# Kernel tuning notes

Measured on AMD Instinct MI355X. Metric: run time of the kernel, lower is better.

Reference implementation:

```python
import jax, jax.numpy as jnp
import numpy as np

N_STATES = 64   # n_dice
N_OBS = 128     # number of distinct roll values (rows of log_likelihood table)
T = 262144      # sequence length


def setup_inputs() -> dict:
    key = jax.random.key(0)
    k1, k2, k3 = jax.random.split(key, 3)
    rolls = jax.random.randint(k1, (T,), 0, N_OBS)
    # torch.nn.init.normal(param, -1, 0.1): mean -1, std 0.1
    transition = jax.random.normal(k2, (N_STATES, N_STATES + 1), dtype=jnp.float32) * 0.1 - 1.0
    # emission log-likelihood table [n_obs, n_states]
    loglik_table = jax.nn.log_softmax(
        jax.random.normal(k3, (N_OBS, N_STATES), dtype=jnp.float32), axis=0)
    return {"rolls": rolls, "transition": transition, "loglik_table": loglik_table}


def reference(rolls, transition, loglik_table):
    """Viterbi decode: returns (path, final_score).

    Faithful to CRF.forward / _viterbi_algorithm, including the quirk that the
    emission vector ll_t is added along the PREVIOUS-state axis
    (roll.view(1,-1) broadcast over prev states), and that the returned path is
    in reverse-time order [s_{T-1}, ..., s_0].
    """
    S = transition.shape[0]
    ll = loglik_table[rolls]                 # [T, S]
    trans = transition[:, :S]                # [S, S]  (next, prev)
    init_delta = transition[:, S] + ll[0]    # [S]     start scores

    def step(delta, ll_t):
        # scores[next, prev] = trans[next, prev] + ll_t[prev] + delta[prev]
        scores = trans + (ll_t + delta)[None, :]
        bp = jnp.argmax(scores, axis=1)      # [S] backpointers
        return jnp.max(scores, axis=1), bp

    final_delta, bps = jax.lax.scan(step, init_delta, ll[1:])  # bps: [T-1, S]
    final_state = jnp.argmax(final_delta)
    final_score = final_delta[final_state]

    def back(state, bp_t):
        prev = bp_t[state]
        return prev, prev

    # reverse-time backtrack; ys[t] = decoded state at time t (t = 0..T-2)
    _, ys = jax.lax.scan(back, final_state, bps, reverse=True)
    path = jnp.concatenate([final_state[None], ys[::-1]])  # [s_{T-1},...,s_0]
    return path, final_score
```

## Files before the change

kernel.cpp:

```cpp
#include <hip/hip_runtime.h>
#include <hip/hip_fp16.h>
#include <stdint.h>

#define T_LEN 262144
#define S 64
#define SP1 65

#define L_FWD 32
#define W_FWD 4
#define NSTEP (L_FWD + W_FWD)
#define C_FWD (T_LEN / L_FWD)

#define LB2 8
#define VB2 8
#define NW (T_LEN / LB2)
#define PITCH (LB2 + 2)

template <int CTRL>
__device__ __forceinline__ float dpp_fmax_step(float v) {
    int t = __builtin_amdgcn_update_dpp(__float_as_int(v), __float_as_int(v),
                                        CTRL, 0xf, 0xf, false);
    return fmaxf(__int_as_float(t), v);
}
template <int CTRL>
__device__ __forceinline__ unsigned int dpp_umin_step(unsigned int v) {
    unsigned int t = (unsigned int)__builtin_amdgcn_update_dpp(
        (int)v, (int)v, CTRL, 0xf, 0xf, false);
    return t < v ? t : v;
}

__device__ __forceinline__ float readlane_f(float v, int lane) {
    return __int_as_float(__builtin_amdgcn_readlane(__float_as_int(v), lane));
}

__device__ __forceinline__ unsigned int pack_key(float a, int j) {
    return (__float_as_uint(a) & 0xFFFFFFC0u) | (unsigned)j;
}

__global__ __launch_bounds__(512, 8) void k1_forward(
    const int* __restrict__ rolls, const float* __restrict__ trans,
    const float* __restrict__ ll,
    unsigned int* __restrict__ bp4, int* __restrict__ wsFinal,
    float* __restrict__ out_score) {
    __shared__ float strans[S * S];
    __shared__ __half sll[128 * S];
    const int tid = threadIdx.x;
    const int lane = tid & 63;
    const int wv = tid >> 6;

    if (blockIdx.x == 0 && tid == 0)
        out_score[0] = 0.0f;

    for (int k = tid; k < S * S; k += 512) {
        int i = k >> 6, j = k & 63;
        strans[(j << 6) | i] = trans[i * SP1 + j];
    }
    for (int k = tid; k < 128 * S; k += 512)
        sll[k] = __float2half(ll[k]);

    float rm = 3.0e38f;
    #pragma unroll
    for (int w = 0; w < S; ++w)
        rm = fminf(rm, trans[lane * SP1 + w]);
    float mc = 3.0e38f;
    #pragma unroll
    for (int i = 0; i < S; ++i)
        mc = fminf(mc, readlane_f(rm, i) - trans[i * SP1 + lane]);
    const float mcol = mc - 0.01f;
    __syncthreads();

    const int c = blockIdx.x * 8 + wv;
    const int t0 = c * L_FWD - W_FWD;

    int vroll = rolls[min(max(t0 + lane, 0), T_LEN - 1)];

    float delta = 0.0f;
    unsigned int pk[8];
    const int lane4 = lane << 0;

    #pragma unroll
    for (int st = 0; st < NSTEP; ++st) {
        int r = __builtin_amdgcn_readlane(vroll, st);
        float llv = __half2float(sll[(r << 6) | lane]);

        float cvec = delta + llv;

        float mxc = cvec;
        mxc = dpp_fmax_step<0x111>(mxc);
        mxc = dpp_fmax_step<0x112>(mxc);
        mxc = dpp_fmax_step<0x114>(mxc);
        mxc = dpp_fmax_step<0x118>(mxc);
        mxc = dpp_fmax_step<0x142>(mxc);
        mxc = dpp_fmax_step<0x143>(mxc);
        float cmax = readlane_f(mxc, 63);

        float thr = cmax + mcol;
        unsigned long long m0 = __ballot(cvec >= thr);

        int j0 = __ffsll(m0) - 1;
        unsigned long long m1 = m0 & (m0 - 1);
        int j1 = m1 ? (__ffsll(m1) - 1) : j0;
        unsigned long long m2 = m1 & (m1 - 1);
        int j2 = m2 ? (__ffsll(m2) - 1) : j0;
        unsigned long long m3 = m2 & (m2 - 1);
        int j3 = m3 ? (__ffsll(m3) - 1) : j0;

        float a0 = strans[(j0 << 6) | lane] + readlane_f(cvec, j0);
        float a1 = strans[(j1 << 6) | lane] + readlane_f(cvec, j1);
        float a2 = strans[(j2 << 6) | lane] + readlane_f(cvec, j2);
        float a3 = strans[(j3 << 6) | lane] + readlane_f(cvec, j3);

        unsigned int m = min(min(pack_key(a0, j0), pack_key(a1, j1)),
                             min(pack_key(a2, j2), pack_key(a3, j3)));

        delta = __uint_as_float(m & 0xFFFFFFC0u);

        if (st >= W_FWD) {
            int q = (st - W_FWD) >> 2, u = (st - W_FWD) & 3;
            if (u == 0) pk[q] = (m & 63u);
            else        pk[q] |= (m & 63u) << (8 * u);
        }
    }

    const int qb = c * (L_FWD / 4);
    #pragma unroll
    for (int q = 0; q < 8; ++q)
        bp4[(unsigned)((qb + q) << 6) | (unsigned)lane] = pk[q];

    if (c == C_FWD - 1) {
        unsigned int key = __float_as_uint(delta) | (unsigned)lane;
        key = dpp_umin_step<0x111>(key);
        key = dpp_umin_step<0x112>(key);
        key = dpp_umin_step<0x114>(key);
        key = dpp_umin_step<0x118>(key);
        key = dpp_umin_step<0x142>(key);
        key = dpp_umin_step<0x143>(key);
        unsigned int kall = (unsigned int)__builtin_amdgcn_readlane((int)key, 63);
        if (lane == 0)
            *wsFinal = (int)(kall & 63u);
    }
    (void)lane4;
}

__global__ __launch_bounds__(256) void k2_backtrack(
    const unsigned int* __restrict__ bp4, const int* __restrict__ wsFinal,
    const int* __restrict__ rolls, const float* __restrict__ trans,
    const float* __restrict__ ll, float* __restrict__ out_path,
    float* __restrict__ out_score) {
    __shared__ int sst[256 * PITCH];
    __shared__ float spart[4];
    const int tid = threadIdx.x;
    const int b = blockIdx.x * 256 + tid;
    const int tlo = b * LB2;
    const int thi = tlo + LB2 - 1;
    int te = thi + VB2;
    int s;
    if (te >= T_LEN - 1) {
        te = T_LEN - 1;
        s = *wsFinal;
    } else {
        s = 0;
    }
    int* row = sst + tid * PITCH;
    #pragma unroll
    for (int u = 0; u < LB2 + VB2 - 1; ++u) {
        int t = te - u;
        if (t > tlo) {
            if (t <= thi + 1) row[t - tlo] = s;
            unsigned int w = bp4[((unsigned)(t >> 2) << 6) | (unsigned)s];
            s = (int)((w >> ((t & 3) << 3)) & 63u);
        }
    }
    row[0] = s;
    __syncthreads();

    #pragma unroll
    for (int u = 0; u < LB2; ++u)
        out_path[T_LEN - 1 - (tlo + u)] = (float)row[u];

    float acc = 0.0f;
    #pragma unroll
    for (int u = 1; u <= LB2; ++u) {
        int t = tlo + u;
        if (t <= T_LEN - 1) {
            int sp = row[u - 1];
            int st = (u == LB2)
                         ? ((tid < 255) ? sst[(tid + 1) * PITCH] : row[LB2])
                         : row[u];
            acc += trans[st * SP1 + sp] + ll[rolls[t] * S + sp];
        }
    }
    if (b == 0) {
        int s0 = row[0];
        acc += trans[s0 * SP1 + S] + ll[rolls[0] * S + s0];
    }

    for (int off = 32; off; off >>= 1)
        acc += __shfl_xor(acc, off);
    if ((tid & 63) == 0) spart[tid >> 6] = acc;
    __syncthreads();
    if (tid == 0)
        atomicAdd(out_score, (spart[0] + spart[1]) + (spart[2] + spart[3]));
}

extern "C" void kernel_launch(void* const* d_in, const int* in_sizes, int n_in,
                              void* d_out, int out_size, void* d_ws, size_t ws_size,
                              hipStream_t stream) {
    const int* rolls = (const int*)d_in[0];
    const float* trans = (const float*)d_in[1];
    const float* ll = (const float*)d_in[2];
    float* out = (float*)d_out;
    char* ws = (char*)d_ws;
    int* wsFinal = (int*)(ws + 8);
    unsigned int* bp4 = (unsigned int*)(ws + 2048);

    k1_forward<<<C_FWD / 8, 512, 0, stream>>>(rolls, trans, ll, bp4, wsFinal,
                                              out + T_LEN);
    k2_backtrack<<<NW / 256, 256, 0, stream>>>(bp4, wsFinal, rolls, trans, ll,
                                               out, out + T_LEN);
}
```

Before: 114.5 us.

## Fuse pairs of Viterbi steps via precomputed per-roll max-plus two-step matrices

Adds a precompute kernel that builds, for each of the 128 roll values, a combined two-step max-plus transition matrix and a per-column pruning threshold. The forward pass then advances two time steps per iteration, halving the sequential chain length, and reads the combined matrices from global memory instead of LDS. The backtrack recovers the skipped intermediate states by an argmax over the middle state. In exchange it adds a 2 MB table built every call, global-memory gathers inside the forward loop, and a wave-wide reduction per recovered state in the backtrack.

```diff
diff --git a/kernel.cpp b/kernel.cpp
--- a/kernel.cpp
+++ b/kernel.cpp
@@ -5,16 +5,14 @@
 #define T_LEN 262144
 #define S 64
 #define SP1 65
-
-#define L_FWD 32
-#define W_FWD 4
-#define NSTEP (L_FWD + W_FWD)
-#define C_FWD (T_LEN / L_FWD)
-
-#define LB2 8
-#define VB2 8
-#define NW (T_LEN / LB2)
-#define PITCH (LB2 + 2)
+#define NCT 131072
+
+#define L_C 16
+#define W_C 4
+#define NSTEP (L_C + W_C)
+#define C_FWD (NCT / L_C)
+
+#define NW2 (T_LEN / 16)
 
 template <int CTRL>
 __device__ __forceinline__ float dpp_fmax_step(float v) {
@@ -28,62 +26,110 @@
         (int)v, (int)v, CTRL, 0xf, 0xf, false);
     return t < v ? t : v;
 }
-
 __device__ __forceinline__ float readlane_f(float v, int lane) {
     return __int_as_float(__builtin_amdgcn_readlane(__float_as_int(v), lane));
 }
-
 __device__ __forceinline__ unsigned int pack_key(float a, int j) {
     return (__float_as_uint(a) & 0xFFFFFFC0u) | (unsigned)j;
 }
-
-__global__ __launch_bounds__(512, 8) void k1_forward(
+__device__ __forceinline__ unsigned int wave_umin(unsigned int key) {
+    key = dpp_umin_step<0x111>(key);
+    key = dpp_umin_step<0x112>(key);
+    key = dpp_umin_step<0x114>(key);
+    key = dpp_umin_step<0x118>(key);
+    key = dpp_umin_step<0x142>(key);
+    key = dpp_umin_step<0x143>(key);
+    return (unsigned int)__builtin_amdgcn_readlane((int)key, 63);
+}
+
+__global__ __launch_bounds__(1024) void k0_m2(
+    const float* __restrict__ trans, const float* __restrict__ ll,
+    float* __restrict__ wsM2col, float* __restrict__ wsMc2,
+    float* __restrict__ out_score) {
+    __shared__ float sR[S * S];
+    __shared__ float sC[S * S];
+    __shared__ float sv[S];
+    __shared__ float sM2[S * S];
+    __shared__ float srm[S];
+    const int r = blockIdx.x, tid = threadIdx.x;
+    const int lane = tid & 63, wv = tid >> 6;
+    for (int k = tid; k < S * S; k += 1024) {
+        float v = trans[(k >> 6) * SP1 + (k & 63)];
+        sR[k] = v;
+        sC[k] = v;
+    }
+    if (tid < S) sv[tid] = ll[r * S + tid];
+    __syncthreads();
+    #pragma unroll
+    for (int ii = 0; ii < 4; ++ii) {
+        int i = wv * 4 + ii;
+        float m = -3.0e38f;
+        for (int k = 0; k < S; ++k) {
+            float tik = sR[(i << 6) | k] + sv[k];
+            m = fmaxf(m, tik + sC[(k << 6) | lane]);
+        }
+        sM2[(i << 6) | lane] = m;
+    }
+    __syncthreads();
+    if (tid < S) {
+        float rm = 3.0e38f;
+        for (int j = 0; j < S; ++j) rm = fminf(rm, sM2[(tid << 6) | j]);
+        srm[tid] = rm;
+    }
+    __syncthreads();
+    if (tid < S) {
+        float mc = 3.0e38f;
+        for (int i = 0; i < S; ++i) mc = fminf(mc, srm[i] - sM2[(i << 6) | tid]);
+        wsMc2[r * S + tid] = mc;
+    }
+    for (int idx = tid; idx < S * S; idx += 1024) {
+        int j = idx >> 6, i = idx & 63;
+        wsM2col[(r << 12) | idx] = sM2[(i << 6) | j];
+    }
+    if (r == 0 && tid == 0) out_score[0] = 0.0f;
+}
+
+__global__ __launch_bounds__(256, 8) void k1_forward(
     const int* __restrict__ rolls, const float* __restrict__ trans,
-    const float* __restrict__ ll,
-    unsigned int* __restrict__ bp4, int* __restrict__ wsFinal,
-    float* __restrict__ out_score) {
-    __shared__ float strans[S * S];
+    const float* __restrict__ ll, const float* __restrict__ wsMc2,
+    const float* __restrict__ wsM2col, unsigned int* __restrict__ bp4,
+    int* __restrict__ wsFinal, unsigned char* __restrict__ bpF) {
     __shared__ __half sll[128 * S];
     const int tid = threadIdx.x;
     const int lane = tid & 63;
     const int wv = tid >> 6;
 
-    if (blockIdx.x == 0 && tid == 0)
-        out_score[0] = 0.0f;
-
-    for (int k = tid; k < S * S; k += 512) {
-        int i = k >> 6, j = k & 63;
-        strans[(j << 6) | i] = trans[i * SP1 + j];
-    }
-    for (int k = tid; k < 128 * S; k += 512)
+    for (int k = tid; k < 128 * S; k += 256)
         sll[k] = __float2half(ll[k]);
-
-    float rm = 3.0e38f;
-    #pragma unroll
-    for (int w = 0; w < S; ++w)
-        rm = fminf(rm, trans[lane * SP1 + w]);
-    float mc = 3.0e38f;
-    #pragma unroll
-    for (int i = 0; i < S; ++i)
-        mc = fminf(mc, readlane_f(rm, i) - trans[i * SP1 + lane]);
-    const float mcol = mc - 0.01f;
-    __syncthreads();
-
-    const int c = blockIdx.x * 8 + wv;
-    const int t0 = c * L_FWD - W_FWD;
-
-    int vroll = rolls[min(max(t0 + lane, 0), T_LEN - 1)];
+    __syncthreads();
+
+    const int c = blockIdx.x * 4 + wv;
+    const int ct0 = c * L_C - W_C;
+
+    int ci = ct0 + lane;
+    int vrO = rolls[min(max(2 * ci + 1, 0), T_LEN - 1)];
+    int vrE = rolls[min(max(2 * ci + 2, 0), T_LEN - 1)];
 
     float delta = 0.0f;
-    unsigned int pk[8];
-    const int lane4 = lane << 0;
+    unsigned int pk[4];
+    float dsave = 0.0f;
+
+    int rO0 = __builtin_amdgcn_readlane(vrO, 0);
+    int rE0 = __builtin_amdgcn_readlane(vrE, 0);
+    float ll_cur = __half2float(sll[(rO0 << 6) | lane]);
+    float mc_cur = wsMc2[(rE0 << 6) | lane];
 
     #pragma unroll
     for (int st = 0; st < NSTEP; ++st) {
-        int r = __builtin_amdgcn_readlane(vroll, st);
-        float llv = __half2float(sll[(r << 6) | lane]);
-
-        float cvec = delta + llv;
+        int rO_n = __builtin_amdgcn_readlane(vrO, st + 1);
+        int rE_n = __builtin_amdgcn_readlane(vrE, st + 1);
+        float ll_nxt = __half2float(sll[(rO_n << 6) | lane]);
+        float mc_nxt = wsMc2[(rE_n << 6) | lane];
+        int rE = __builtin_amdgcn_readlane(vrE, st);
+
+        if (st == NSTEP - 1) dsave = delta;
+
+        float cvec = delta + ll_cur;
 
         float mxc = cvec;
         mxc = dpp_fmax_step<0x111>(mxc);
@@ -94,7 +140,7 @@
         mxc = dpp_fmax_step<0x143>(mxc);
         float cmax = readlane_f(mxc, 63);
 
-        float thr = cmax + mcol;
+        float thr = cmax + mc_cur;
         unsigned long long m0 = __ballot(cvec >= thr);
 
         int j0 = __ffsll(m0) - 1;
@@ -105,99 +151,126 @@
         unsigned long long m3 = m2 & (m2 - 1);
         int j3 = m3 ? (__ffsll(m3) - 1) : j0;
 
-        float a0 = strans[(j0 << 6) | lane] + readlane_f(cvec, j0);
-        float a1 = strans[(j1 << 6) | lane] + readlane_f(cvec, j1);
-        float a2 = strans[(j2 << 6) | lane] + readlane_f(cvec, j2);
-        float a3 = strans[(j3 << 6) | lane] + readlane_f(cvec, j3);
+        const float* base = wsM2col + ((size_t)rE << 12);
+        float a0 = base[(j0 << 6) | lane] + readlane_f(cvec, j0);
+        float a1 = base[(j1 << 6) | lane] + readlane_f(cvec, j1);
+        float a2 = base[(j2 << 6) | lane] + readlane_f(cvec, j2);
+        float a3 = base[(j3 << 6) | lane] + readlane_f(cvec, j3);
 
         unsigned int m = min(min(pack_key(a0, j0), pack_key(a1, j1)),
                              min(pack_key(a2, j2), pack_key(a3, j3)));
 
         delta = __uint_as_float(m & 0xFFFFFFC0u);
 
-        if (st >= W_FWD) {
-            int q = (st - W_FWD) >> 2, u = (st - W_FWD) & 3;
+        if (st >= W_C) {
+            int q = (st - W_C) >> 2, u = (st - W_C) & 3;
             if (u == 0) pk[q] = (m & 63u);
             else        pk[q] |= (m & 63u) << (8 * u);
         }
-    }
-
-    const int qb = c * (L_FWD / 4);
-    #pragma unroll
-    for (int q = 0; q < 8; ++q)
+        ll_cur = ll_nxt;
+        mc_cur = mc_nxt;
+    }
+
+    const int qb = c * 4;
+    #pragma unroll
+    for (int q = 0; q < 4; ++q)
         bp4[(unsigned)((qb + q) << 6) | (unsigned)lane] = pk[q];
 
     if (c == C_FWD - 1) {
-        unsigned int key = __float_as_uint(delta) | (unsigned)lane;
-        key = dpp_umin_step<0x111>(key);
-        key = dpp_umin_step<0x112>(key);
-        key = dpp_umin_step<0x114>(key);
-        key = dpp_umin_step<0x118>(key);
-        key = dpp_umin_step<0x142>(key);
-        key = dpp_umin_step<0x143>(key);
-        unsigned int kall = (unsigned int)__builtin_amdgcn_readlane((int)key, 63);
+        int rF = rolls[T_LEN - 1];
+        float cvF = dsave + __half2float(sll[(rF << 6) | lane]);
+        unsigned int mbest = 0xFFFFFFFFu;
+        for (int j = 0; j < S; ++j) {
+            float a = trans[lane * SP1 + j] + readlane_f(cvF, j);
+            mbest = min(mbest, pack_key(a, j));
+        }
+        bpF[lane] = (unsigned char)(mbest & 63u);
+        float deltaF = __uint_as_float(mbest & 0xFFFFFFC0u);
+        unsigned int kall = wave_umin(pack_key(deltaF, lane));
         if (lane == 0)
             *wsFinal = (int)(kall & 63u);
     }
-    (void)lane4;
 }
 
 __global__ __launch_bounds__(256) void k2_backtrack(
     const unsigned int* __restrict__ bp4, const int* __restrict__ wsFinal,
-    const int* __restrict__ rolls, const float* __restrict__ trans,
-    const float* __restrict__ ll, float* __restrict__ out_path,
-    float* __restrict__ out_score) {
-    __shared__ int sst[256 * PITCH];
+    const unsigned char* __restrict__ bpF, const int* __restrict__ rolls,
+    const float* __restrict__ trans, const float* __restrict__ ll,
+    float* __restrict__ out_path, float* __restrict__ out_score) {
+    __shared__ float sR[S * S];
+    __shared__ float sC[S * S];
+    __shared__ int swin[4][18];
     __shared__ float spart[4];
     const int tid = threadIdx.x;
-    const int b = blockIdx.x * 256 + tid;
-    const int tlo = b * LB2;
-    const int thi = tlo + LB2 - 1;
-    int te = thi + VB2;
-    int s;
-    if (te >= T_LEN - 1) {
-        te = T_LEN - 1;
-        s = *wsFinal;
+    const int lane = tid & 63;
+    const int wv = tid >> 6;
+
+    for (int k = tid; k < S * S; k += 256) {
+        int i = k >> 6, j = k & 63;
+        float v = trans[i * SP1 + j];
+        sR[(i << 6) | j] = v;
+        sC[(j << 6) | i] = v;
+    }
+    __syncthreads();
+
+    const int w = blockIdx.x * 4 + wv;
+    const int tlo = w * 16;
+    const int ctlo = w * 8;
+
+    int cte, s;
+    if (ctlo + 16 >= NCT) {
+        cte = NCT - 1;
+        s = (int)bpF[*wsFinal];
     } else {
+        cte = ctlo + 16;
         s = 0;
     }
-    int* row = sst + tid * PITCH;
-    #pragma unroll
-    for (int u = 0; u < LB2 + VB2 - 1; ++u) {
-        int t = te - u;
-        if (t > tlo) {
-            if (t <= thi + 1) row[t - tlo] = s;
-            unsigned int w = bp4[((unsigned)(t >> 2) << 6) | (unsigned)s];
-            s = (int)((w >> ((t & 3) << 3)) & 63u);
-        }
-    }
-    row[0] = s;
-    __syncthreads();
-
-    #pragma unroll
-    for (int u = 0; u < LB2; ++u)
-        out_path[T_LEN - 1 - (tlo + u)] = (float)row[u];
-
-    float acc = 0.0f;
-    #pragma unroll
-    for (int u = 1; u <= LB2; ++u) {
-        int t = tlo + u;
+    if (cte <= ctlo + 8 && lane == 0)
+        swin[wv][2 * (cte - ctlo)] = s;
+    for (int ct = cte - 1; ct >= ctlo; --ct) {
+        unsigned int wd = bp4[((unsigned)(ct >> 2) << 6) | (unsigned)s];
+        s = (int)((wd >> ((ct & 3) << 3)) & 63u);
+        if (ct <= ctlo + 8 && lane == 0)
+            swin[wv][2 * (ct - ctlo)] = s;
+    }
+
+    int rq = rolls[min(2 * (ctlo + lane) + 2, T_LEN - 1)];
+    #pragma unroll
+    for (int q = 0; q < 8; ++q) {
+        int ct = ctlo + q;
+        int i = swin[wv][2 * q + 2];
+        int j = swin[wv][2 * q];
+        int sodd;
+        if (ct >= NCT - 1) {
+            sodd = *wsFinal;
+        } else {
+            int r = __builtin_amdgcn_readlane(rq, q);
+            float val = sR[(i << 6) | lane] + ll[(r << 6) + lane] +
+                        sC[(j << 6) | lane];
+            unsigned int kall = wave_umin(pack_key(val, lane));
+            sodd = (int)(kall & 63u);
+        }
+        if (lane == 0) swin[wv][2 * q + 1] = sodd;
+    }
+
+    if (lane < 16)
+        out_path[T_LEN - 1 - (tlo + lane)] = (float)swin[wv][lane];
+
+    float term = 0.0f;
+    if (lane < 16) {
+        int t = tlo + 1 + lane;
         if (t <= T_LEN - 1) {
-            int sp = row[u - 1];
-            int st = (u == LB2)
-                         ? ((tid < 255) ? sst[(tid + 1) * PITCH] : row[LB2])
-                         : row[u];
-            acc += trans[st * SP1 + sp] + ll[rolls[t] * S + sp];
-        }
-    }
-    if (b == 0) {
-        int s0 = row[0];
-        acc += trans[s0 * SP1 + S] + ll[rolls[0] * S + s0];
-    }
-
+            int sp = swin[wv][lane];
+            int st_ = swin[wv][lane + 1];
+            term = trans[st_ * SP1 + sp] + ll[rolls[t] * S + sp];
+        }
+    } else if (lane == 16 && w == 0) {
+        int s0 = swin[wv][0];
+        term = trans[s0 * SP1 + S] + ll[rolls[0] * S + s0];
+    }
     for (int off = 32; off; off >>= 1)
-        acc += __shfl_xor(acc, off);
-    if ((tid & 63) == 0) spart[tid >> 6] = acc;
+        term += __shfl_xor(term, off);
+    if (lane == 0) spart[wv] = term;
     __syncthreads();
     if (tid == 0)
         atomicAdd(out_score, (spart[0] + spart[1]) + (spart[2] + spart[3]));
@@ -212,10 +285,14 @@
     float* out = (float*)d_out;
     char* ws = (char*)d_ws;
     int* wsFinal = (int*)(ws + 8);
-    unsigned int* bp4 = (unsigned int*)(ws + 2048);
-
-    k1_forward<<<C_FWD / 8, 512, 0, stream>>>(rolls, trans, ll, bp4, wsFinal,
-                                              out + T_LEN);
-    k2_backtrack<<<NW / 256, 256, 0, stream>>>(bp4, wsFinal, rolls, trans, ll,
-                                               out, out + T_LEN);
-}
+    unsigned char* bpF = (unsigned char*)(ws + 128);
+    float* wsMc2 = (float*)(ws + 4096);
+    float* wsM2col = (float*)(ws + 64 * 1024);
+    unsigned int* bp4 = (unsigned int*)(ws + 4 * 1024 * 1024);
+
+    k0_m2<<<128, 1024, 0, stream>>>(trans, ll, wsM2col, wsMc2, out + T_LEN);
+    k1_forward<<<C_FWD / 4, 256, 0, stream>>>(rolls, trans, ll, wsMc2, wsM2col,
+                                              bp4, wsFinal, bpF);
+    k2_backtrack<<<NW2 / 4, 256, 0, stream>>>(bp4, wsFinal, bpF, rolls, trans,
+                                              ll, out, out + T_LEN);
+}
```

Result: slower. 216.7 us (+89.2%).
